# Performance work log

Hardware: AMD Instinct MI355X
Metric: run time of the kernel (lower is better)

Reference implementation:

```python
import jax, jax.numpy as jnp
import numpy as np

B = 2_000_000
CLAMP_MIN = 0.01
NORM_EPS = 1e-5


def setup_inputs() -> dict:
    key = jax.random.key(0)
    F = jax.random.normal(key, (B, 3, 3), dtype=jnp.float32)
    # learned scalar parameters (per init_kwargs)
    youngs_modulus_log = jnp.asarray(13.0, dtype=jnp.float32)
    poissons_ratio = jnp.asarray(0.3, dtype=jnp.float32)
    yield_stress = jnp.asarray(3000.0, dtype=jnp.float32)
    return {
        "F": F,
        "youngs_modulus_log": youngs_modulus_log,
        "poissons_ratio": poissons_ratio,
        "yield_stress": yield_stress,
    }


def reference(F, youngs_modulus_log, poissons_ratio, yield_stress):
    # von-Mises return mapping on singular values of the deformation gradient
    youngs_modulus = jnp.exp(youngs_modulus_log)
    mu = youngs_modulus / (2.0 * (1.0 + poissons_ratio))  # shear modulus

    # batched 3x3 SVD: U (B,3,3), sigma (B,3), Vh (B,3,3)
    U, sigma, Vh = jnp.linalg.svd(F, full_matrices=False)

    sigma = jnp.maximum(sigma, CLAMP_MIN)
    epsilon = jnp.log(sigma)                                  # (B,3) Hencky strain
    epsilon_trace = jnp.sum(epsilon, axis=1, keepdims=True)   # (B,1)
    epsilon_bar = epsilon - epsilon_trace / 3.0               # deviatoric strain
    epsilon_bar_norm = jnp.linalg.norm(epsilon_bar, axis=1, keepdims=True) + NORM_EPS

    delta_gamma = epsilon_bar_norm - yield_stress / (2.0 * mu)  # (B,1)
    yield_epsilon = epsilon - (delta_gamma / epsilon_bar_norm) * epsilon_bar
    yield_sigma = jnp.exp(yield_epsilon)

    sigma = jnp.where(delta_gamma > 0.0, yield_sigma, sigma)  # (B,3)

    # F_corrected = U @ diag(sigma) @ Vh, fused without materializing diag
    F_corrected = jnp.einsum("bij,bj,bjk->bik", U, sigma, Vh)
    return F_corrected
```

## Files before the change

kernel.cpp:

```cpp
#include <hip/hip_runtime.h>
#include <math.h>

#define TPB 256
#define NQ 2
#define CHUNK (TPB * NQ)
#define CH_F (CHUNK * 9)
#define CH_F4 (CH_F / 4)

typedef float v2  __attribute__((ext_vector_type(2)));
typedef int   v2i __attribute__((ext_vector_type(2)));
typedef float f4u __attribute__((ext_vector_type(4), aligned(4)));

static __device__ __forceinline__ v2 V2(float x){ v2 r; r.x=x; r.y=x; return r; }
static __device__ __forceinline__ v2 vfma(v2 a, v2 b, v2 c){ return __builtin_elementwise_fma(a, b, c); }
static __device__ __forceinline__ v2 vmax(v2 a, v2 b){ return __builtin_elementwise_max(a, b); }
static __device__ __forceinline__ v2 vabs(v2 a){ return __builtin_elementwise_abs(a); }
static __device__ __forceinline__ v2 vcps(v2 a, v2 b){ return __builtin_elementwise_copysign(a, b); }

static __device__ __forceinline__ v2 rsq2(v2 x){ v2 r; r.x=__builtin_amdgcn_rsqf(x.x);  r.y=__builtin_amdgcn_rsqf(x.y);  return r; }
static __device__ __forceinline__ v2 rcp2(v2 x){ v2 r; r.x=__builtin_amdgcn_rcpf(x.x);  r.y=__builtin_amdgcn_rcpf(x.y);  return r; }
static __device__ __forceinline__ v2 sqt2(v2 x){ v2 r; r.x=__builtin_amdgcn_sqrtf(x.x); r.y=__builtin_amdgcn_sqrtf(x.y); return r; }
static __device__ __forceinline__ v2 lg22(v2 x){ v2 r; r.x=__builtin_amdgcn_logf(x.x);  r.y=__builtin_amdgcn_logf(x.y);  return r; }
static __device__ __forceinline__ v2 ex22(v2 x){ v2 r; r.x=__builtin_amdgcn_exp2f(x.x); r.y=__builtin_amdgcn_exp2f(x.y); return r; }

static __device__ __forceinline__ v2 vsel(v2i m, v2 a, v2 b){
  v2i ai = __builtin_bit_cast(v2i, a), bi = __builtin_bit_cast(v2i, b);
  return __builtin_bit_cast(v2, bi ^ ((ai ^ bi) & m));
}

static __device__ __forceinline__ void gl_lds16(const float* g, float* l){
  __builtin_amdgcn_global_load_lds(
      (const __attribute__((address_space(1))) void*)g,
      (__attribute__((address_space(3))) void*)l, 16, 0, 0);
}

__device__ __forceinline__ void jcs2(v2 app_in, v2 aqq_in, v2 apq,
                                     v2& c, v2& s,
                                     v2& app_out, v2& aqq_out)
{
  v2 d    = (aqq_in - app_in) * 0.5f;
  v2 r2   = vmax(vfma(d, d, apq * apq), V2(1e-30f));
  v2 invh = rsq2(r2);
  v2 h    = r2 * invh;
  v2 sg   = vcps(V2(1.0f), d);
  v2 ch   = h + vabs(d);
  v2 sh   = apq * sg;
  v2 w    = rsq2(vfma(ch, ch, sh * sh));
  c = ch * w;
  s = sh * w;
  v2 hs = h * sg;
  v2 m  = app_in + d;
  app_out = m - hs;
  aqq_out = m + hs;
}

__device__ __forceinline__ void jrot(v2& app, v2& aqq, v2& apq,
                                     v2& apk, v2& aqk,
                                     v2& vp0, v2& vp1, v2& vp2,
                                     v2& vq0, v2& vq1, v2& vq2)
{
  v2 c, s;
  jcs2(app, aqq, apq, c, s, app, aqq);
  apq = V2(0.0f);
  v2 pk = apk, qk = aqk;
  apk = c * pk - s * qk;
  aqk = s * pk + c * qk;
  v2 v;
  v = vp0; vp0 = c*v - s*vq0; vq0 = s*v + c*vq0;
  v = vp1; vp1 = c*v - s*vq1; vq1 = s*v + c*vq1;
  v = vp2; vp2 = c*v - s*vq2; vq2 = s*v + c*vq2;
}

#define CSWAP(li, lj, a0, a1, a2, b0, b1, b2)                                   \
  do {                                                                          \
    v2i _m = (li) < (lj);                                                       \
    v2 _t;                                                                      \
    _t = vsel(_m,(lj),(li)); (lj) = vsel(_m,(li),(lj)); (li) = _t;              \
    _t = vsel(_m,(b0),(a0)); (b0) = vsel(_m,(a0),(b0)); (a0) = _t;              \
    _t = vsel(_m,(b1),(a1)); (b1) = vsel(_m,(a1),(b1)); (a1) = _t;              \
    _t = vsel(_m,(b2),(a2)); (b2) = vsel(_m,(a2),(b2)); (a2) = _t;              \
  } while (0)

__global__ __launch_bounds__(TPB) void plastic_svd_kernel(
    const float* __restrict__ F,
    const float* __restrict__ p_yml,
    const float* __restrict__ p_nu,
    const float* __restrict__ p_ys,
    float* __restrict__ out,
    int nmat, int nchunks)
{
  __shared__ float lds[2][CH_F];
  const int tid  = threadIdx.x;
  const int totF  = nmat * 9;
  const int totF4 = totF >> 2;

  const float mu_s = __builtin_amdgcn_exp2f(p_yml[0] * 1.44269504f) *
                     __builtin_amdgcn_rcpf(2.0f * (1.0f + p_nu[0]));
  const float qy_s = p_ys[0] * 0.5f * __builtin_amdgcn_rcpf(mu_s);
  const v2 qy = V2(qy_s);

  auto STAGE = [&](int t, int b){
    const int f4base = t * CH_F4;
    #pragma unroll
    for (int k = 0; k < 5; ++k) {
      int i4  = k * TPB + tid;
      int gi4 = f4base + i4;
      if (i4 < CH_F4 && gi4 < totF4)
        gl_lds16(F + gi4 * 4, &lds[b][i4 * 4]);
    }
    int e0 = totF4 << 2;
    int e  = e0 + tid;
    if (e < totF) {
      int fb = t * CH_F;
      if (e >= fb && e < fb + CH_F) lds[b][e - fb] = F[e];
    }
  };

  int cur = 0;
  STAGE(blockIdx.x, 0);
  __syncthreads();

  for (int t = blockIdx.x; t < nchunks; t += gridDim.x) {
    int tn = t + gridDim.x;
    if (tn < nchunks) STAGE(tn, cur ^ 1);

    const int mbase = t * CHUNK;
    const int mi0 = mbase + tid;
    const int mi1 = mbase + TPB + tid;
    const float* mA = &lds[cur][tid * 9];
    const float* mB = &lds[cur][(TPB + tid) * 9];

    v2 s00, s11, s22, s01, s02, s12;
    {
      v2 f00,f01,f02,f10,f11,f12,f20,f21,f22;
      f00.x=mA[0]; f01.x=mA[1]; f02.x=mA[2];
      f10.x=mA[3]; f11.x=mA[4]; f12.x=mA[5];
      f20.x=mA[6]; f21.x=mA[7]; f22.x=mA[8];
      f00.y=mB[0]; f01.y=mB[1]; f02.y=mB[2];
      f10.y=mB[3]; f11.y=mB[4]; f12.y=mB[5];
      f20.y=mB[6]; f21.y=mB[7]; f22.y=mB[8];
      s00 = f00*f00 + f10*f10 + f20*f20;
      s11 = f01*f01 + f11*f11 + f21*f21;
      s22 = f02*f02 + f12*f12 + f22*f22;
      s01 = f00*f01 + f10*f11 + f20*f21;
      s02 = f00*f02 + f10*f12 + f20*f22;
      s12 = f01*f02 + f11*f12 + f21*f22;
    }

    v2 v00,v01,v02,v10,v11,v12,v20,v21,v22;
    v2 c, s;

    jcs2(s00, s11, s01, c, s, s00, s11);
    { v2 pk = s02, qk = s12; s02 = c*pk - s*qk; s12 = s*pk + c*qk; }
    v00 = c;  v01 = s;
    v10 = -s; v11 = c;
    s01 = V2(0.0f);
    jcs2(s00, s22, s02, c, s, s00, s22);
    { v2 pk = s01, qk = s12; s01 = c*pk - s*qk; s12 = s*pk + c*qk; }
    v02 = s * v00; v12 = s * v10; v22 = c;
    v00 = c * v00; v10 = c * v10; v20 = -s;
    v21 = V2(0.0f);
    s02 = V2(0.0f);
    jrot(s11, s22, s12, s01, s02, v01, v11, v21, v02, v12, v22);
    jrot(s00, s11, s01, s02, s12, v00, v10, v20, v01, v11, v21);
    jrot(s00, s22, s02, s01, s12, v00, v10, v20, v02, v12, v22);
    jrot(s11, s22, s12, s01, s02, v01, v11, v21, v02, v12, v22);
    jrot(s00, s11, s01, s02, s12, v00, v10, v20, v01, v11, v21);
    jrot(s00, s22, s02, s01, s12, v00, v10, v20, v02, v12, v22);
    jcs2(s11, s22, s12, c, s, s11, s22);
    { v2 v;
      v = v01; v01 = c*v - s*v02; v02 = s*v + c*v02;
      v = v11; v11 = c*v - s*v12; v12 = s*v + c*v12;
      v = v21; v21 = c*v - s*v22; v22 = s*v + c*v22; }

    v2 l0 = s00, l1 = s11, l2 = s22;
    CSWAP(l0, l1, v00, v10, v20, v01, v11, v21);
    CSWAP(l1, l2, v01, v11, v21, v02, v12, v22);
    CSWAP(l0, l1, v00, v10, v20, v01, v11, v21);

    v2 f00,f01,f02,f10,f11,f12,f20,f21,f22;
    f00.x=mA[0]; f01.x=mA[1]; f02.x=mA[2];
    f10.x=mA[3]; f11.x=mA[4]; f12.x=mA[5];
    f20.x=mA[6]; f21.x=mA[7]; f22.x=mA[8];
    f00.y=mB[0]; f01.y=mB[1]; f02.y=mB[2];
    f10.y=mB[3]; f11.y=mB[4]; f12.y=mB[5];
    f20.y=mB[6]; f21.y=mB[7]; f22.y=mB[8];

    v2 w0x = f00*v00 + f01*v10 + f02*v20;
    v2 w0y = f10*v00 + f11*v10 + f12*v20;
    v2 w0z = f20*v00 + f21*v10 + f22*v20;
    v2 n0sq = w0x*w0x + w0y*w0y + w0z*w0z;
    v2 inv0 = rsq2(vmax(n0sq, V2(1e-30f)));
    v2 u0x = w0x*inv0, u0y = w0y*inv0, u0z = w0z*inv0;

    v2 w1x = f00*v01 + f01*v11 + f02*v21;
    v2 w1y = f10*v01 + f11*v11 + f12*v21;
    v2 w1z = f20*v01 + f21*v11 + f22*v21;
    v2 n1sq_pre = w1x*w1x + w1y*w1y + w1z*w1z;
    v2 d01 = w1x*u0x + w1y*u0y + w1z*u0z;
    w1x = w1x - d01*u0x; w1y = w1y - d01*u0y; w1z = w1z - d01*u0z;
    v2 n1sq = w1x*w1x + w1y*w1y + w1z*w1z;
    v2 inv1 = rsq2(vmax(n1sq, V2(1e-30f)));
    v2 u1x = w1x*inv1, u1y = w1y*inv1, u1z = w1z*inv1;

    v2 u2x = u0y*u1z - u0z*u1y;
    v2 u2y = u0z*u1x - u0x*u1z;
    v2 u2z = u0x*u1y - u0y*u1x;
    v2 w2x = f00*v02 + f01*v12 + f02*v22;
    v2 w2y = f10*v02 + f11*v12 + f12*v22;
    v2 w2z = f20*v02 + f21*v12 + f22*v22;
    v2 s2d = u2x*w2x + u2y*w2y + u2z*w2z;
    v2 sg = vcps(V2(1.0f), s2d);
    v2 sig2 = vabs(s2d);
    u2x = u2x * sg; u2y = u2y * sg; u2z = u2z * sg;

    v2 e0 = lg22(vmax(n0sq,     V2(1e-4f))) * 0.5f;
    v2 e1 = lg22(vmax(n1sq_pre, V2(1e-4f))) * 0.5f;
    v2 e2 = lg22(vmax(sig2,     V2(0.01f)));
    v2 m3 = (e0 + e1 + e2) * (1.0f / 3.0f);
    v2 b0 = e0 - m3, b1 = e1 - m3, b2 = e2 - m3;
    v2 bn = sqt2(b0*b0 + b1*b1 + b2*b2) * 0.69314718f + V2(1e-5f);
    v2 r = vmax(bn - qy, V2(0.0f)) * rcp2(bn);
    v2 c0 = ex22(e0 - r * b0);
    v2 c1 = ex22(e1 - r * b1);
    v2 c2 = ex22(e2 - r * b2);

    v2 a0x = c0*u0x, a0y = c0*u0y, a0z = c0*u0z;
    v2 a1x = c1*u1x, a1y = c1*u1y, a1z = c1*u1z;
    v2 a2x = c2*u2x, a2y = c2*u2y, a2z = c2*u2z;

    v2 o00 = a0x*v00 + a1x*v01 + a2x*v02;
    v2 o01 = a0x*v10 + a1x*v11 + a2x*v12;
    v2 o02 = a0x*v20 + a1x*v21 + a2x*v22;
    v2 o10 = a0y*v00 + a1y*v01 + a2y*v02;
    v2 o11 = a0y*v10 + a1y*v11 + a2y*v12;
    v2 o12 = a0y*v20 + a1y*v21 + a2y*v22;
    v2 o20 = a0z*v00 + a1z*v01 + a2z*v02;
    v2 o21 = a0z*v10 + a1z*v11 + a2z*v12;
    v2 o22 = a0z*v20 + a1z*v21 + a2z*v22;

    if (mi0 < nmat) {
      float* p = out + mi0 * 9;
      f4u a = {o00.x, o01.x, o02.x, o10.x};
      f4u b = {o11.x, o12.x, o20.x, o21.x};
      *(f4u*)(p)     = a;
      *(f4u*)(p + 4) = b;
      p[8] = o22.x;
    }
    if (mi1 < nmat) {
      float* p = out + mi1 * 9;
      f4u a = {o00.y, o01.y, o02.y, o10.y};
      f4u b = {o11.y, o12.y, o20.y, o21.y};
      *(f4u*)(p)     = a;
      *(f4u*)(p + 4) = b;
      p[8] = o22.y;
    }

    __syncthreads();
    cur ^= 1;
  }
}

extern "C" void kernel_launch(void* const* d_in, const int* in_sizes, int n_in,
                              void* d_out, int out_size, void* d_ws, size_t ws_size,
                              hipStream_t stream) {
  const float* F     = (const float*)d_in[0];
  const float* p_yml = (const float*)d_in[1];
  const float* p_nu  = (const float*)d_in[2];
  const float* p_ys  = (const float*)d_in[3];
  float* out = (float*)d_out;

  const int nmat = in_sizes[0] / 9;
  const int nchunks = (nmat + CHUNK - 1) / CHUNK;
  int G = (nchunks + 3) / 4;
  if (G > 1024) G = 1024;
  if (G < 1) G = 1;
  hipLaunchKernelGGL(plastic_svd_kernel, dim3(G), dim3(TPB), 0, stream,
                     F, p_yml, p_nu, p_ys, out, nmat, nchunks);
}
```

Measured before the change: 38.53 us.

## Replace persistent LDS-staged pipeline with one-shot grid loading adjacent matrix pairs directly

Drops the persistent grid-stride loop with double-buffered global_load_lds staging. Each thread now loads two adjacent matrices directly from global memory with 8-byte vector loads and writes its outputs with 8-byte stores. LDS is used only to park the F values across the Jacobi sweep, which should cut register pressure, and the grid is one block per 512 matrices. This removes block-wide barriers and staging overhead, but per-thread loads are strided by 72 bytes, so coalescing is worse than with the contiguous staged copy, and prefetch overlap now depends only on occupancy.

```diff
diff --git a/kernel.cpp b/kernel.cpp
--- a/kernel.cpp
+++ b/kernel.cpp
@@ -4,12 +4,10 @@
 #define TPB 256
 #define NQ 2
 #define CHUNK (TPB * NQ)
-#define CH_F (CHUNK * 9)
-#define CH_F4 (CH_F / 4)
 
 typedef float v2  __attribute__((ext_vector_type(2)));
 typedef int   v2i __attribute__((ext_vector_type(2)));
-typedef float f4u __attribute__((ext_vector_type(4), aligned(4)));
+typedef float f2g __attribute__((ext_vector_type(2), aligned(8)));
 
 static __device__ __forceinline__ v2 V2(float x){ v2 r; r.x=x; r.y=x; return r; }
 static __device__ __forceinline__ v2 vfma(v2 a, v2 b, v2 c){ return __builtin_elementwise_fma(a, b, c); }
@@ -26,12 +24,6 @@
 static __device__ __forceinline__ v2 vsel(v2i m, v2 a, v2 b){
   v2i ai = __builtin_bit_cast(v2i, a), bi = __builtin_bit_cast(v2i, b);
   return __builtin_bit_cast(v2, bi ^ ((ai ^ bi) & m));
-}
-
-static __device__ __forceinline__ void gl_lds16(const float* g, float* l){
-  __builtin_amdgcn_global_load_lds(
-      (const __attribute__((address_space(1))) void*)g,
-      (__attribute__((address_space(3))) void*)l, 16, 0, 0);
 }
 
 __device__ __forceinline__ void jcs2(v2 app_in, v2 aqq_in, v2 apq,
@@ -87,177 +79,152 @@
     const float* __restrict__ p_nu,
     const float* __restrict__ p_ys,
     float* __restrict__ out,
-    int nmat, int nchunks)
+    int nmat)
 {
-  __shared__ float lds[2][CH_F];
-  const int tid  = threadIdx.x;
-  const int totF  = nmat * 9;
-  const int totF4 = totF >> 2;
+  __shared__ v2 sf[9][TPB];
+  const int tid = threadIdx.x;
+  const int u   = blockIdx.x * TPB + tid;
+  const int m0  = 2 * u;
+  if (m0 >= nmat) return;
+  const bool full = (m0 + 1 < nmat);
+
+  v2 f00,f01,f02,f10,f11,f12,f20,f21,f22;
+  if (full) {
+    const f2g* gp = (const f2g*)(F + (size_t)m0 * 9);
+    f2g r0=gp[0], r1=gp[1], r2=gp[2], r3=gp[3], r4=gp[4],
+        r5=gp[5], r6=gp[6], r7=gp[7], r8=gp[8];
+    f00.x=r0.x; f00.y=r4.y;
+    f01.x=r0.y; f01.y=r5.x;
+    f02.x=r1.x; f02.y=r5.y;
+    f10.x=r1.y; f10.y=r6.x;
+    f11.x=r2.x; f11.y=r6.y;
+    f12.x=r2.y; f12.y=r7.x;
+    f20.x=r3.x; f20.y=r7.y;
+    f21.x=r3.y; f21.y=r8.x;
+    f22.x=r4.x; f22.y=r8.y;
+  } else {
+    const float* p = F + (size_t)m0 * 9;
+    f00=V2(p[0]); f01=V2(p[1]); f02=V2(p[2]);
+    f10=V2(p[3]); f11=V2(p[4]); f12=V2(p[5]);
+    f20=V2(p[6]); f21=V2(p[7]); f22=V2(p[8]);
+  }
 
   const float mu_s = __builtin_amdgcn_exp2f(p_yml[0] * 1.44269504f) *
                      __builtin_amdgcn_rcpf(2.0f * (1.0f + p_nu[0]));
   const float qy_s = p_ys[0] * 0.5f * __builtin_amdgcn_rcpf(mu_s);
   const v2 qy = V2(qy_s);
 
-  auto STAGE = [&](int t, int b){
-    const int f4base = t * CH_F4;
-    #pragma unroll
-    for (int k = 0; k < 5; ++k) {
-      int i4  = k * TPB + tid;
-      int gi4 = f4base + i4;
-      if (i4 < CH_F4 && gi4 < totF4)
-        gl_lds16(F + gi4 * 4, &lds[b][i4 * 4]);
-    }
-    int e0 = totF4 << 2;
-    int e  = e0 + tid;
-    if (e < totF) {
-      int fb = t * CH_F;
-      if (e >= fb && e < fb + CH_F) lds[b][e - fb] = F[e];
-    }
-  };
-
-  int cur = 0;
-  STAGE(blockIdx.x, 0);
-  __syncthreads();
-
-  for (int t = blockIdx.x; t < nchunks; t += gridDim.x) {
-    int tn = t + gridDim.x;
-    if (tn < nchunks) STAGE(tn, cur ^ 1);
-
-    const int mbase = t * CHUNK;
-    const int mi0 = mbase + tid;
-    const int mi1 = mbase + TPB + tid;
-    const float* mA = &lds[cur][tid * 9];
-    const float* mB = &lds[cur][(TPB + tid) * 9];
-
-    v2 s00, s11, s22, s01, s02, s12;
-    {
-      v2 f00,f01,f02,f10,f11,f12,f20,f21,f22;
-      f00.x=mA[0]; f01.x=mA[1]; f02.x=mA[2];
-      f10.x=mA[3]; f11.x=mA[4]; f12.x=mA[5];
-      f20.x=mA[6]; f21.x=mA[7]; f22.x=mA[8];
-      f00.y=mB[0]; f01.y=mB[1]; f02.y=mB[2];
-      f10.y=mB[3]; f11.y=mB[4]; f12.y=mB[5];
-      f20.y=mB[6]; f21.y=mB[7]; f22.y=mB[8];
-      s00 = f00*f00 + f10*f10 + f20*f20;
-      s11 = f01*f01 + f11*f11 + f21*f21;
-      s22 = f02*f02 + f12*f12 + f22*f22;
-      s01 = f00*f01 + f10*f11 + f20*f21;
-      s02 = f00*f02 + f10*f12 + f20*f22;
-      s12 = f01*f02 + f11*f12 + f21*f22;
-    }
-
-    v2 v00,v01,v02,v10,v11,v12,v20,v21,v22;
-    v2 c, s;
-
-    jcs2(s00, s11, s01, c, s, s00, s11);
-    { v2 pk = s02, qk = s12; s02 = c*pk - s*qk; s12 = s*pk + c*qk; }
-    v00 = c;  v01 = s;
-    v10 = -s; v11 = c;
-    s01 = V2(0.0f);
-    jcs2(s00, s22, s02, c, s, s00, s22);
-    { v2 pk = s01, qk = s12; s01 = c*pk - s*qk; s12 = s*pk + c*qk; }
-    v02 = s * v00; v12 = s * v10; v22 = c;
-    v00 = c * v00; v10 = c * v10; v20 = -s;
-    v21 = V2(0.0f);
-    s02 = V2(0.0f);
-    jrot(s11, s22, s12, s01, s02, v01, v11, v21, v02, v12, v22);
-    jrot(s00, s11, s01, s02, s12, v00, v10, v20, v01, v11, v21);
-    jrot(s00, s22, s02, s01, s12, v00, v10, v20, v02, v12, v22);
-    jrot(s11, s22, s12, s01, s02, v01, v11, v21, v02, v12, v22);
-    jrot(s00, s11, s01, s02, s12, v00, v10, v20, v01, v11, v21);
-    jrot(s00, s22, s02, s01, s12, v00, v10, v20, v02, v12, v22);
-    jcs2(s11, s22, s12, c, s, s11, s22);
-    { v2 v;
-      v = v01; v01 = c*v - s*v02; v02 = s*v + c*v02;
-      v = v11; v11 = c*v - s*v12; v12 = s*v + c*v12;
-      v = v21; v21 = c*v - s*v22; v22 = s*v + c*v22; }
-
-    v2 l0 = s00, l1 = s11, l2 = s22;
-    CSWAP(l0, l1, v00, v10, v20, v01, v11, v21);
-    CSWAP(l1, l2, v01, v11, v21, v02, v12, v22);
-    CSWAP(l0, l1, v00, v10, v20, v01, v11, v21);
-
-    v2 f00,f01,f02,f10,f11,f12,f20,f21,f22;
-    f00.x=mA[0]; f01.x=mA[1]; f02.x=mA[2];
-    f10.x=mA[3]; f11.x=mA[4]; f12.x=mA[5];
-    f20.x=mA[6]; f21.x=mA[7]; f22.x=mA[8];
-    f00.y=mB[0]; f01.y=mB[1]; f02.y=mB[2];
-    f10.y=mB[3]; f11.y=mB[4]; f12.y=mB[5];
-    f20.y=mB[6]; f21.y=mB[7]; f22.y=mB[8];
-
-    v2 w0x = f00*v00 + f01*v10 + f02*v20;
-    v2 w0y = f10*v00 + f11*v10 + f12*v20;
-    v2 w0z = f20*v00 + f21*v10 + f22*v20;
-    v2 n0sq = w0x*w0x + w0y*w0y + w0z*w0z;
-    v2 inv0 = rsq2(vmax(n0sq, V2(1e-30f)));
-    v2 u0x = w0x*inv0, u0y = w0y*inv0, u0z = w0z*inv0;
-
-    v2 w1x = f00*v01 + f01*v11 + f02*v21;
-    v2 w1y = f10*v01 + f11*v11 + f12*v21;
-    v2 w1z = f20*v01 + f21*v11 + f22*v21;
-    v2 n1sq_pre = w1x*w1x + w1y*w1y + w1z*w1z;
-    v2 d01 = w1x*u0x + w1y*u0y + w1z*u0z;
-    w1x = w1x - d01*u0x; w1y = w1y - d01*u0y; w1z = w1z - d01*u0z;
-    v2 n1sq = w1x*w1x + w1y*w1y + w1z*w1z;
-    v2 inv1 = rsq2(vmax(n1sq, V2(1e-30f)));
-    v2 u1x = w1x*inv1, u1y = w1y*inv1, u1z = w1z*inv1;
-
-    v2 u2x = u0y*u1z - u0z*u1y;
-    v2 u2y = u0z*u1x - u0x*u1z;
-    v2 u2z = u0x*u1y - u0y*u1x;
-    v2 w2x = f00*v02 + f01*v12 + f02*v22;
-    v2 w2y = f10*v02 + f11*v12 + f12*v22;
-    v2 w2z = f20*v02 + f21*v12 + f22*v22;
-    v2 s2d = u2x*w2x + u2y*w2y + u2z*w2z;
-    v2 sg = vcps(V2(1.0f), s2d);
-    v2 sig2 = vabs(s2d);
-    u2x = u2x * sg; u2y = u2y * sg; u2z = u2z * sg;
-
-    v2 e0 = lg22(vmax(n0sq,     V2(1e-4f))) * 0.5f;
-    v2 e1 = lg22(vmax(n1sq_pre, V2(1e-4f))) * 0.5f;
-    v2 e2 = lg22(vmax(sig2,     V2(0.01f)));
-    v2 m3 = (e0 + e1 + e2) * (1.0f / 3.0f);
-    v2 b0 = e0 - m3, b1 = e1 - m3, b2 = e2 - m3;
-    v2 bn = sqt2(b0*b0 + b1*b1 + b2*b2) * 0.69314718f + V2(1e-5f);
-    v2 r = vmax(bn - qy, V2(0.0f)) * rcp2(bn);
-    v2 c0 = ex22(e0 - r * b0);
-    v2 c1 = ex22(e1 - r * b1);
-    v2 c2 = ex22(e2 - r * b2);
-
-    v2 a0x = c0*u0x, a0y = c0*u0y, a0z = c0*u0z;
-    v2 a1x = c1*u1x, a1y = c1*u1y, a1z = c1*u1z;
-    v2 a2x = c2*u2x, a2y = c2*u2y, a2z = c2*u2z;
-
-    v2 o00 = a0x*v00 + a1x*v01 + a2x*v02;
-    v2 o01 = a0x*v10 + a1x*v11 + a2x*v12;
-    v2 o02 = a0x*v20 + a1x*v21 + a2x*v22;
-    v2 o10 = a0y*v00 + a1y*v01 + a2y*v02;
-    v2 o11 = a0y*v10 + a1y*v11 + a2y*v12;
-    v2 o12 = a0y*v20 + a1y*v21 + a2y*v22;
-    v2 o20 = a0z*v00 + a1z*v01 + a2z*v02;
-    v2 o21 = a0z*v10 + a1z*v11 + a2z*v12;
-    v2 o22 = a0z*v20 + a1z*v21 + a2z*v22;
-
-    if (mi0 < nmat) {
-      float* p = out + mi0 * 9;
-      f4u a = {o00.x, o01.x, o02.x, o10.x};
-      f4u b = {o11.x, o12.x, o20.x, o21.x};
-      *(f4u*)(p)     = a;
-      *(f4u*)(p + 4) = b;
-      p[8] = o22.x;
-    }
-    if (mi1 < nmat) {
-      float* p = out + mi1 * 9;
-      f4u a = {o00.y, o01.y, o02.y, o10.y};
-      f4u b = {o11.y, o12.y, o20.y, o21.y};
-      *(f4u*)(p)     = a;
-      *(f4u*)(p + 4) = b;
-      p[8] = o22.y;
-    }
-
-    __syncthreads();
-    cur ^= 1;
+  v2 s00 = f00*f00 + f10*f10 + f20*f20;
+  v2 s11 = f01*f01 + f11*f11 + f21*f21;
+  v2 s22 = f02*f02 + f12*f12 + f22*f22;
+  v2 s01 = f00*f01 + f10*f11 + f20*f21;
+  v2 s02 = f00*f02 + f10*f12 + f20*f22;
+  v2 s12 = f01*f02 + f11*f12 + f21*f22;
+
+  sf[0][tid]=f00; sf[1][tid]=f01; sf[2][tid]=f02;
+  sf[3][tid]=f10; sf[4][tid]=f11; sf[5][tid]=f12;
+  sf[6][tid]=f20; sf[7][tid]=f21; sf[8][tid]=f22;
+
+  v2 v00,v01,v02,v10,v11,v12,v20,v21,v22;
+  v2 c, s;
+
+  jcs2(s00, s11, s01, c, s, s00, s11);
+  { v2 pk = s02, qk = s12; s02 = c*pk - s*qk; s12 = s*pk + c*qk; }
+  v00 = c;  v01 = s;
+  v10 = -s; v11 = c;
+  s01 = V2(0.0f);
+  jcs2(s00, s22, s02, c, s, s00, s22);
+  { v2 pk = s01, qk = s12; s01 = c*pk - s*qk; s12 = s*pk + c*qk; }
+  v02 = s * v00; v12 = s * v10; v22 = c;
+  v00 = c * v00; v10 = c * v10; v20 = -s;
+  v21 = V2(0.0f);
+  s02 = V2(0.0f);
+  jrot(s11, s22, s12, s01, s02, v01, v11, v21, v02, v12, v22);
+  jrot(s00, s11, s01, s02, s12, v00, v10, v20, v01, v11, v21);
+  jrot(s00, s22, s02, s01, s12, v00, v10, v20, v02, v12, v22);
+  jrot(s11, s22, s12, s01, s02, v01, v11, v21, v02, v12, v22);
+  jrot(s00, s11, s01, s02, s12, v00, v10, v20, v01, v11, v21);
+  jrot(s00, s22, s02, s01, s12, v00, v10, v20, v02, v12, v22);
+  jcs2(s11, s22, s12, c, s, s11, s22);
+  { v2 v;
+    v = v01; v01 = c*v - s*v02; v02 = s*v + c*v02;
+    v = v11; v11 = c*v - s*v12; v12 = s*v + c*v12;
+    v = v21; v21 = c*v - s*v22; v22 = s*v + c*v22; }
+
+  v2 l0 = s00, l1 = s11, l2 = s22;
+  CSWAP(l0, l1, v00, v10, v20, v01, v11, v21);
+  CSWAP(l1, l2, v01, v11, v21, v02, v12, v22);
+  CSWAP(l0, l1, v00, v10, v20, v01, v11, v21);
+
+  f00=sf[0][tid]; f01=sf[1][tid]; f02=sf[2][tid];
+  f10=sf[3][tid]; f11=sf[4][tid]; f12=sf[5][tid];
+  f20=sf[6][tid]; f21=sf[7][tid]; f22=sf[8][tid];
+
+  v2 w0x = f00*v00 + f01*v10 + f02*v20;
+  v2 w0y = f10*v00 + f11*v10 + f12*v20;
+  v2 w0z = f20*v00 + f21*v10 + f22*v20;
+  v2 n0sq = w0x*w0x + w0y*w0y + w0z*w0z;
+  v2 inv0 = rsq2(vmax(n0sq, V2(1e-30f)));
+  v2 u0x = w0x*inv0, u0y = w0y*inv0, u0z = w0z*inv0;
+
+  v2 w1x = f00*v01 + f01*v11 + f02*v21;
+  v2 w1y = f10*v01 + f11*v11 + f12*v21;
+  v2 w1z = f20*v01 + f21*v11 + f22*v21;
+  v2 n1sq_pre = w1x*w1x + w1y*w1y + w1z*w1z;
+  v2 d01 = w1x*u0x + w1y*u0y + w1z*u0z;
+  w1x = w1x - d01*u0x; w1y = w1y - d01*u0y; w1z = w1z - d01*u0z;
+  v2 n1sq = w1x*w1x + w1y*w1y + w1z*w1z;
+  v2 inv1 = rsq2(vmax(n1sq, V2(1e-30f)));
+  v2 u1x = w1x*inv1, u1y = w1y*inv1, u1z = w1z*inv1;
+
+  v2 u2x = u0y*u1z - u0z*u1y;
+  v2 u2y = u0z*u1x - u0x*u1z;
+  v2 u2z = u0x*u1y - u0y*u1x;
+  v2 w2x = f00*v02 + f01*v12 + f02*v22;
+  v2 w2y = f10*v02 + f11*v12 + f12*v22;
+  v2 w2z = f20*v02 + f21*v12 + f22*v22;
+  v2 s2d = u2x*w2x + u2y*w2y + u2z*w2z;
+  v2 sg = vcps(V2(1.0f), s2d);
+  v2 sig2 = vabs(s2d);
+  u2x = u2x * sg; u2y = u2y * sg; u2z = u2z * sg;
+
+  v2 e0 = lg22(vmax(n0sq,     V2(1e-4f))) * 0.5f;
+  v2 e1 = lg22(vmax(n1sq_pre, V2(1e-4f))) * 0.5f;
+  v2 e2 = lg22(vmax(sig2,     V2(0.01f)));
+  v2 m3 = (e0 + e1 + e2) * (1.0f / 3.0f);
+  v2 b0 = e0 - m3, b1 = e1 - m3, b2 = e2 - m3;
+  v2 bn = sqt2(b0*b0 + b1*b1 + b2*b2) * 0.69314718f + V2(1e-5f);
+  v2 r = vmax(bn - qy, V2(0.0f)) * rcp2(bn);
+  v2 c0 = ex22(e0 - r * b0);
+  v2 c1 = ex22(e1 - r * b1);
+  v2 c2 = ex22(e2 - r * b2);
+
+  v2 a0x = c0*u0x, a0y = c0*u0y, a0z = c0*u0z;
+  v2 a1x = c1*u1x, a1y = c1*u1y, a1z = c1*u1z;
+  v2 a2x = c2*u2x, a2y = c2*u2y, a2z = c2*u2z;
+
+  v2 o00 = a0x*v00 + a1x*v01 + a2x*v02;
+  v2 o01 = a0x*v10 + a1x*v11 + a2x*v12;
+  v2 o02 = a0x*v20 + a1x*v21 + a2x*v22;
+  v2 o10 = a0y*v00 + a1y*v01 + a2y*v02;
+  v2 o11 = a0y*v10 + a1y*v11 + a2y*v12;
+  v2 o12 = a0y*v20 + a1y*v21 + a2y*v22;
+  v2 o20 = a0z*v00 + a1z*v01 + a2z*v02;
+  v2 o21 = a0z*v10 + a1z*v11 + a2z*v12;
+  v2 o22 = a0z*v20 + a1z*v21 + a2z*v22;
+
+  if (full) {
+    f2g* op = (f2g*)(out + (size_t)m0 * 9);
+    f2g w0={o00.x,o01.x}, w1={o02.x,o10.x}, w2={o11.x,o12.x},
+        w3={o20.x,o21.x}, w4={o22.x,o00.y}, w5={o01.y,o02.y},
+        w6={o10.y,o11.y}, w7={o12.y,o20.y}, w8={o21.y,o22.y};
+    op[0]=w0; op[1]=w1; op[2]=w2; op[3]=w3; op[4]=w4;
+    op[5]=w5; op[6]=w6; op[7]=w7; op[8]=w8;
+  } else {
+    float* p = out + (size_t)m0 * 9;
+    p[0]=o00.x; p[1]=o01.x; p[2]=o02.x;
+    p[3]=o10.x; p[4]=o11.x; p[5]=o12.x;
+    p[6]=o20.x; p[7]=o21.x; p[8]=o22.x;
   }
 }
 
@@ -271,10 +238,7 @@
   float* out = (float*)d_out;
 
   const int nmat = in_sizes[0] / 9;
-  const int nchunks = (nmat + CHUNK - 1) / CHUNK;
-  int G = (nchunks + 3) / 4;
-  if (G > 1024) G = 1024;
-  if (G < 1) G = 1;
-  hipLaunchKernelGGL(plastic_svd_kernel, dim3(G), dim3(TPB), 0, stream,
-                     F, p_yml, p_nu, p_ys, out, nmat, nchunks);
-}
+  const int nblocks = (nmat + CHUNK - 1) / CHUNK;
+  hipLaunchKernelGGL(plastic_svd_kernel, dim3(nblocks), dim3(TPB), 0, stream,
+                     F, p_yml, p_nu, p_ys, out, nmat);
+}
```

Result: slower. 42.84 us (+11.2%).
